# Performance work log

Hardware: AMD Instinct MI355X
Metric: run time of the kernel (lower is better)

## Reference

```python
import jax, jax.numpy as jnp
import numpy as np
import math

B, L, C = 16, 4096, 512
SPARSE_RATIO = 0.6
NUM_KEEP = math.ceil(L * SPARSE_RATIO)  # 2458


def setup_inputs() -> dict:
    key = jax.random.key(0)
    k1, k2, k3 = jax.random.split(key, 3)
    return {
        "tokens": jax.random.normal(k1, (B, L, C), dtype=jnp.float32),
        "attention_x": jax.random.normal(k2, (B, L), dtype=jnp.float32),
        "attention_y": jax.random.normal(k3, (B, L), dtype=jnp.float32),
    }


def reference(tokens, attention_x, attention_y):
    eps = 1e-6
    # coverage-fused score: alpha = sigmoid(1 - mean(ay)/mean(ax))
    coverage = attention_y.mean(axis=1) / (attention_x.mean(axis=1) + eps)  # [B]
    alpha = jax.nn.sigmoid(1.0 - coverage)                                  # [B]
    beta = 1.0 - alpha
    score = alpha[:, None] * attention_x + beta[:, None] * attention_y      # [B, L]

    # full descending sort of scores
    order = jnp.argsort(-score, axis=1)                                     # [B, L]
    score_sort = jnp.take_along_axis(score, order, axis=1)                  # [B, L]

    keep_policy = order[:, :NUM_KEEP]                                       # [B, K]
    non_keep_policy = order[:, NUM_KEEP:]                                   # [B, L-K]

    # scatter 1s at kept positions
    batch_idx = jnp.arange(B)[:, None]
    score_mask = jnp.zeros_like(score).at[batch_idx, keep_policy].set(1.0)  # [B, L]

    # gather kept / pruned tokens
    select_tokens = jnp.take_along_axis(tokens, keep_policy[:, :, None], axis=1)      # [B, K, C]
    non_tokens = jnp.take_along_axis(tokens, non_keep_policy[:, :, None], axis=1)     # [B, L-K, C]

    # softmax-weighted merge of pruned tokens into one extra token
    non_keep_score = jax.nn.softmax(score_sort[:, NUM_KEEP:], axis=1)[:, :, None]     # [B, L-K, 1]
    extra_token = jnp.sum(non_tokens * non_keep_score, axis=1, keepdims=True)         # [B, 1, C]

    return select_tokens, extra_token, score_mask
```

## Files before the change

### kernel.cpp

```cpp
#include <hip/hip_runtime.h>
#include <math.h>

#define NB 16
#define NL 4096
#define NC 512
#define NC4 128
#define NKEEP 2458
#define KEEPB 76
#define NTAILB 52

typedef float f32x4 __attribute__((ext_vector_type(4)));


__global__ void __launch_bounds__(1024) k_front(const float* __restrict__ ax,
                                                const float* __restrict__ ay,
                                                unsigned long long* __restrict__ key,
                                                float* __restrict__ alpha,
                                                float* __restrict__ beta,
                                                unsigned* __restrict__ smaxu) {
  int b = blockIdx.x;
  int tid = threadIdx.x;
  __shared__ float s_ab[2];
  __shared__ unsigned redmaxu[16];
  if (tid < 64) {
    int lane = tid;
    float sx = 0.0f, sy = 0.0f;
    if (lane < 32) {
      const float* px = ax + b * NL + lane * 128;
      const float* py = ay + b * NL + lane * 128;
      float r[8], q[8];
#pragma unroll
      for (int j = 0; j < 8; ++j) { r[j] = px[j]; q[j] = py[j]; }
      for (int i = 8; i < 128; i += 8) {
#pragma unroll
        for (int j = 0; j < 8; ++j) {
          r[j] = __fadd_rn(r[j], px[i + j]);
          q[j] = __fadd_rn(q[j], py[i + j]);
        }
      }
      sx = __fadd_rn(__fadd_rn(__fadd_rn(r[0], r[1]), __fadd_rn(r[2], r[3])),
                     __fadd_rn(__fadd_rn(r[4], r[5]), __fadd_rn(r[6], r[7])));
      sy = __fadd_rn(__fadd_rn(__fadd_rn(q[0], q[1]), __fadd_rn(q[2], q[3])),
                     __fadd_rn(__fadd_rn(q[4], q[5]), __fadd_rn(q[6], q[7])));
    }
#pragma unroll
    for (int m = 1; m <= 16; m <<= 1) {
      sx = __fadd_rn(sx, __shfl_xor(sx, m, 64));
      sy = __fadd_rn(sy, __shfl_xor(sy, m, 64));
    }
    if (lane == 0) {
      float mx = __fdiv_rn(sx, 4096.0f);
      float my = __fdiv_rn(sy, 4096.0f);
      float cov = __fdiv_rn(my, __fadd_rn(mx, 1e-6f));
      float z = __fsub_rn(1.0f, cov);
      double a = 1.0 / (1.0 + exp(-(double)z));
      float af = (float)a;
      alpha[b] = af;
      beta[b] = __fsub_rn(1.0f, af);
      s_ab[0] = af;
      s_ab[1] = __fsub_rn(1.0f, af);
    }
  }
  __syncthreads();
  float af = s_ab[0], bf = s_ab[1];
  unsigned m = 0;
#pragma unroll
  for (int p = 0; p < 4; ++p) {
    int l = p * 1024 + tid;
    int idx = b * NL + l;
    float s = __fadd_rn(__fmul_rn(af, ax[idx]), __fmul_rn(bf, ay[idx]));
    unsigned u = __float_as_uint(s);
    unsigned su = u ^ ((u & 0x80000000u) ? 0xFFFFFFFFu : 0x80000000u);
    key[idx] = ((unsigned long long)(~su) << 32) | (unsigned)l;
    m = (su > m) ? su : m;
  }
#pragma unroll
  for (int d = 1; d < 64; d <<= 1) {
    unsigned o = (unsigned)__shfl_xor((int)m, d, 64);
    m = (o > m) ? o : m;
  }
  if ((tid & 63) == 0) redmaxu[tid >> 6] = m;
  __syncthreads();
  if (tid == 0) {
    unsigned M = redmaxu[0];
#pragma unroll
    for (int k = 1; k < 16; ++k) M = (redmaxu[k] > M) ? redmaxu[k] : M;
    smaxu[b] = M;
  }
}

__global__ void __launch_bounds__(256) k_sort(const unsigned long long* __restrict__ key,
                                              unsigned long long* __restrict__ skey) {
  __shared__ unsigned long long lk[512];
  int b = blockIdx.y;
  int c = blockIdx.x;
  int t = threadIdx.x;
  const unsigned long long* kb = key + (size_t)b * NL + c * 512;
  lk[t] = kb[t];
  lk[t + 256] = kb[t + 256];
  __syncthreads();
  for (int k = 2; k <= 512; k <<= 1) {
    for (int j = k >> 1; j > 0; j >>= 1) {
#pragma unroll
      for (int e = 0; e < 2; ++e) {
        int i = t + e * 256;
        int l = i ^ j;
        if (l > i) {
          unsigned long long a = lk[i], bb = lk[l];
          bool up = ((i & k) == 0);
          if ((a > bb) == up) { lk[i] = bb; lk[l] = a; }
        }
      }
      __syncthreads();
    }
  }
  unsigned long long* sb = skey + ((size_t)b * 8 + c) * 512;
  sb[t] = lk[t];
  sb[t + 256] = lk[t + 256];
}

__global__ void __launch_bounds__(1024) k_mid(const float* __restrict__ ax,
                                              const float* __restrict__ ay,
                                              const float* __restrict__ alpha,
                                              const float* __restrict__ beta,
                                              const unsigned long long* __restrict__ skey,
                                              const unsigned* __restrict__ smaxu,
                                              float* __restrict__ w,
                                              float* __restrict__ mask_out,
                                              int* __restrict__ order,
                                              float* __restrict__ Zpart) {
  __shared__ unsigned long long lsk[4096];
  __shared__ float zred[16];
  int bx = blockIdx.x;
  int b = bx >> 2;
  int q = bx & 3;
  int t = threadIdx.x;
  const unsigned long long* sb = skey + (size_t)b * NL;
#pragma unroll
  for (int k = 0; k < 4; ++k) lsk[k * 1024 + t] = sb[k * 1024 + t];
  __syncthreads();

  int l = q * 1024 + t;
  int gid = b * NL + l;
  float s = __fadd_rn(__fmul_rn(alpha[b], ax[gid]), __fmul_rn(beta[b], ay[gid]));
  unsigned u = __float_as_uint(s);
  unsigned su = u ^ ((u & 0x80000000u) ? 0xFFFFFFFFu : 0x80000000u);
  unsigned long long ki = ((unsigned long long)(~su) << 32) | (unsigned)l;

  int r = 0;
#pragma unroll
  for (int c = 0; c < 8; ++c) {
    const unsigned long long* base = lsk + c * 512;
    int pos = 0;
#pragma unroll
    for (int step = 512; step >= 1; step >>= 1) {
      int cand = pos + step;
      if (cand <= 512 && base[cand - 1] < ki) pos = cand;
    }
    r += pos;
  }

  mask_out[gid] = (r < NKEEP) ? 1.0f : 0.0f;
  unsigned SU = smaxu[b];
  float smax = (SU & 0x80000000u) ? __uint_as_float(SU ^ 0x80000000u)
                                  : __uint_as_float(~SU);
  float wi = (r >= NKEEP) ? expf(s - smax) : 0.0f;
  w[gid] = wi;
  order[b * NL + r] = l;

  float zs = wi;
#pragma unroll
  for (int d = 1; d < 64; d <<= 1) zs += __shfl_xor(zs, d, 64);
  if ((t & 63) == 0) zred[t >> 6] = zs;
  __syncthreads();
  if (t == 0) {
    float z = 0.0f;
#pragma unroll
    for (int k = 0; k < 16; ++k) z += zred[k];
    Zpart[bx] = z;
  }
}

__global__ void __launch_bounds__(256) k_perm(const f32x4* __restrict__ tok,
                                              const int* __restrict__ order,
                                              const float* __restrict__ w,
                                              f32x4* __restrict__ sel,
                                              f32x4* __restrict__ partial) {
  int b = blockIdx.y;
  int bx = blockIdx.x;
  int p0 = bx * 32;
  int tid = threadIdx.x;
  int col = tid & 127;
  int g = tid >> 7;
  __shared__ int ssrc[32];
  __shared__ float swt[32];
  __shared__ float accsh[512];
  if (tid < 32) {
    int p = p0 + tid;
    int src = order[b * NL + p];
    ssrc[tid] = src;
    swt[tid] = w[b * NL + src];
  }
  __syncthreads();

  const f32x4* tb = tok + (size_t)b * NL * NC4 + col;
  f32x4 v[16];
#pragma unroll
  for (int k = 0; k < 16; ++k)
    v[k] = tb[(size_t)ssrc[g * 16 + k] * NC4];

  f32x4* sb = sel + (size_t)b * NKEEP * NC4 + col;
  float a0 = 0.f, a1 = 0.f, a2 = 0.f, a3 = 0.f;
#pragma unroll
  for (int k = 0; k < 16; ++k) {
    int p = p0 + g * 16 + k;
    if (p < NKEEP) {
      sb[(size_t)p * NC4] = v[k];
    } else {
      float wk = swt[g * 16 + k];
      a0 = fmaf(wk, v[k].x, a0);
      a1 = fmaf(wk, v[k].y, a1);
      a2 = fmaf(wk, v[k].z, a2);
      a3 = fmaf(wk, v[k].w, a3);
    }
  }

  if (bx >= KEEPB) {
    if (g == 1) {
      accsh[col * 4 + 0] = a0; accsh[col * 4 + 1] = a1;
      accsh[col * 4 + 2] = a2; accsh[col * 4 + 3] = a3;
    }
    __syncthreads();
    if (g == 0) {
      f32x4 o;
      o.x = a0 + accsh[col * 4 + 0];
      o.y = a1 + accsh[col * 4 + 1];
      o.z = a2 + accsh[col * 4 + 2];
      o.w = a3 + accsh[col * 4 + 3];
      partial[(size_t)(b * NTAILB + (bx - KEEPB)) * 128 + col] = o;
    }
  }
}

__global__ void __launch_bounds__(512) k_back(const float* __restrict__ partial,
                                              const float* __restrict__ Zpart,
                                              float* __restrict__ extra) {
  int b = blockIdx.x;
  int c = threadIdx.x;
  float Zb = 0.0f;
#pragma unroll
  for (int k = 0; k < 4; ++k) Zb += Zpart[b * 4 + k];
  const float* p = partial + (size_t)b * NTAILB * 512 + c;
  float a0 = 0.f, a1 = 0.f, a2 = 0.f, a3 = 0.f;
#pragma unroll
  for (int j = 0; j < NTAILB; j += 4) {
    a0 += p[(size_t)(j + 0) * 512];
    a1 += p[(size_t)(j + 1) * 512];
    a2 += p[(size_t)(j + 2) * 512];
    a3 += p[(size_t)(j + 3) * 512];
  }
  extra[b * NC + c] = ((a0 + a1) + (a2 + a3)) / Zb;
}

extern "C" void kernel_launch(void* const* d_in, const int* in_sizes, int n_in,
                              void* d_out, int out_size, void* d_ws, size_t ws_size,
                              hipStream_t stream) {
  (void)in_sizes; (void)n_in; (void)out_size; (void)ws_size;
  const f32x4* tok = (const f32x4*)d_in[0];
  const float* ax = (const float*)d_in[1];
  const float* ay = (const float*)d_in[2];

  unsigned long long* key = (unsigned long long*)d_ws;
  unsigned long long* skey = (unsigned long long*)((char*)d_ws + 524288);
  float* w = (float*)((char*)d_ws + 1048576);
  int* order = (int*)((char*)d_ws + 1310720);
  f32x4* partial = (f32x4*)((char*)d_ws + 1572864);
  float* scalars = (float*)((char*)d_ws + 3407872);
  float* alpha = scalars;
  float* beta = scalars + 16;
  unsigned* smaxu = (unsigned*)(scalars + 32);
  float* Zpart = scalars + 48;

  float* out = (float*)d_out;
  f32x4* sel = (f32x4*)out;
  float* extra = out + (size_t)NB * NKEEP * NC;
  float* mask = extra + (size_t)NB * NC;

  k_front<<<NB, 1024, 0, stream>>>(ax, ay, key, alpha, beta, smaxu);
  k_sort<<<dim3(8, NB), 256, 0, stream>>>(key, skey);
  k_mid<<<64, 1024, 0, stream>>>(ax, ay, alpha, beta, skey, smaxu, w, mask, order, Zpart);
  k_perm<<<dim3(128, NB), 256, 0, stream>>>(tok, order, w, sel, partial);
  k_back<<<NB, 512, 0, stream>>>((const float*)partial, Zpart, extra);
}
```

Baseline: 67.55 us.

## Fuse score computation into sort kernel and recompute alpha/max in mid kernel

Removes the separate k_front kernel. Each sort block now recomputes the per-batch alpha/beta from the attention means and builds its keys directly in shared memory, which drops a kernel launch and the global key round trip. The mid kernel recomputes alpha and takes the score max from the heads of the sorted chunks instead of a stored reduction. It also runs 128 blocks of 512 threads instead of 64 of 1024. In exchange the mean reduction is repeated in every block (8x per batch in each kernel), which adds redundant reads of ax and ay.

```diff
diff --git a/kernel.cpp b/kernel.cpp
--- a/kernel.cpp
+++ b/kernel.cpp
@@ -12,18 +12,17 @@
 typedef float f32x4 __attribute__((ext_vector_type(4)));
 
 
-__global__ void __launch_bounds__(1024) k_front(const float* __restrict__ ax,
-                                                const float* __restrict__ ay,
-                                                unsigned long long* __restrict__ key,
-                                                float* __restrict__ alpha,
-                                                float* __restrict__ beta,
-                                                unsigned* __restrict__ smaxu) {
-  int b = blockIdx.x;
-  int tid = threadIdx.x;
+__global__ void __launch_bounds__(256) k_sort(const float* __restrict__ ax,
+                                              const float* __restrict__ ay,
+                                              unsigned long long* __restrict__ skey) {
+  __shared__ unsigned long long lk[512];
   __shared__ float s_ab[2];
-  __shared__ unsigned redmaxu[16];
-  if (tid < 64) {
-    int lane = tid;
+  int b = blockIdx.y;
+  int c = blockIdx.x;
+  int t = threadIdx.x;
+
+  if (t < 64) {
+    int lane = t;
     float sx = 0.0f, sy = 0.0f;
     if (lane < 32) {
       const float* px = ax + b * NL + lane * 128;
@@ -55,50 +54,24 @@
       float z = __fsub_rn(1.0f, cov);
       double a = 1.0 / (1.0 + exp(-(double)z));
       float af = (float)a;
-      alpha[b] = af;
-      beta[b] = __fsub_rn(1.0f, af);
       s_ab[0] = af;
       s_ab[1] = __fsub_rn(1.0f, af);
     }
   }
   __syncthreads();
   float af = s_ab[0], bf = s_ab[1];
-  unsigned m = 0;
-#pragma unroll
-  for (int p = 0; p < 4; ++p) {
-    int l = p * 1024 + tid;
+
+#pragma unroll
+  for (int e = 0; e < 2; ++e) {
+    int l = c * 512 + t + e * 256;
     int idx = b * NL + l;
     float s = __fadd_rn(__fmul_rn(af, ax[idx]), __fmul_rn(bf, ay[idx]));
     unsigned u = __float_as_uint(s);
     unsigned su = u ^ ((u & 0x80000000u) ? 0xFFFFFFFFu : 0x80000000u);
-    key[idx] = ((unsigned long long)(~su) << 32) | (unsigned)l;
-    m = (su > m) ? su : m;
-  }
-#pragma unroll
-  for (int d = 1; d < 64; d <<= 1) {
-    unsigned o = (unsigned)__shfl_xor((int)m, d, 64);
-    m = (o > m) ? o : m;
-  }
-  if ((tid & 63) == 0) redmaxu[tid >> 6] = m;
-  __syncthreads();
-  if (tid == 0) {
-    unsigned M = redmaxu[0];
-#pragma unroll
-    for (int k = 1; k < 16; ++k) M = (redmaxu[k] > M) ? redmaxu[k] : M;
-    smaxu[b] = M;
-  }
-}
-
-__global__ void __launch_bounds__(256) k_sort(const unsigned long long* __restrict__ key,
-                                              unsigned long long* __restrict__ skey) {
-  __shared__ unsigned long long lk[512];
-  int b = blockIdx.y;
-  int c = blockIdx.x;
-  int t = threadIdx.x;
-  const unsigned long long* kb = key + (size_t)b * NL + c * 512;
-  lk[t] = kb[t];
-  lk[t + 256] = kb[t + 256];
-  __syncthreads();
+    lk[t + e * 256] = ((unsigned long long)(~su) << 32) | (unsigned)l;
+  }
+  __syncthreads();
+
   for (int k = 2; k <= 512; k <<= 1) {
     for (int j = k >> 1; j > 0; j >>= 1) {
 #pragma unroll
@@ -119,30 +92,76 @@
   sb[t + 256] = lk[t + 256];
 }
 
-__global__ void __launch_bounds__(1024) k_mid(const float* __restrict__ ax,
-                                              const float* __restrict__ ay,
-                                              const float* __restrict__ alpha,
-                                              const float* __restrict__ beta,
-                                              const unsigned long long* __restrict__ skey,
-                                              const unsigned* __restrict__ smaxu,
-                                              float* __restrict__ w,
-                                              float* __restrict__ mask_out,
-                                              int* __restrict__ order,
-                                              float* __restrict__ Zpart) {
+__global__ void __launch_bounds__(512) k_mid(const float* __restrict__ ax,
+                                             const float* __restrict__ ay,
+                                             const unsigned long long* __restrict__ skey,
+                                             float* __restrict__ w,
+                                             float* __restrict__ mask_out,
+                                             int* __restrict__ order,
+                                             float* __restrict__ Zpart) {
   __shared__ unsigned long long lsk[4096];
-  __shared__ float zred[16];
+  __shared__ float zred[8];
   int bx = blockIdx.x;
-  int b = bx >> 2;
-  int q = bx & 3;
+  int b = bx >> 3;
+  int q = bx & 7;
   int t = threadIdx.x;
   const unsigned long long* sb = skey + (size_t)b * NL;
 #pragma unroll
-  for (int k = 0; k < 4; ++k) lsk[k * 1024 + t] = sb[k * 1024 + t];
-  __syncthreads();
-
-  int l = q * 1024 + t;
+  for (int k = 0; k < 8; ++k) lsk[k * 512 + t] = sb[k * 512 + t];
+  __syncthreads();
+
+  unsigned long long kmin = lsk[0];
+#pragma unroll
+  for (int c = 1; c < 8; ++c) {
+    unsigned long long h = lsk[c * 512];
+    kmin = (h < kmin) ? h : kmin;
+  }
+  unsigned su0 = ~(unsigned)(kmin >> 32);
+  float smax = (su0 & 0x80000000u) ? __uint_as_float(su0 ^ 0x80000000u)
+                                   : __uint_as_float(~su0);
+
+  int l = q * 512 + t;
   int gid = b * NL + l;
-  float s = __fadd_rn(__fmul_rn(alpha[b], ax[gid]), __fmul_rn(beta[b], ay[gid]));
+  __shared__ float s_ab[2];
+  if (t < 64) {
+    int lane = t;
+    float sx = 0.0f, sy = 0.0f;
+    if (lane < 32) {
+      const float* px = ax + b * NL + lane * 128;
+      const float* py = ay + b * NL + lane * 128;
+      float r[8], qq[8];
+#pragma unroll
+      for (int j = 0; j < 8; ++j) { r[j] = px[j]; qq[j] = py[j]; }
+      for (int i = 8; i < 128; i += 8) {
+#pragma unroll
+        for (int j = 0; j < 8; ++j) {
+          r[j] = __fadd_rn(r[j], px[i + j]);
+          qq[j] = __fadd_rn(qq[j], py[i + j]);
+        }
+      }
+      sx = __fadd_rn(__fadd_rn(__fadd_rn(r[0], r[1]), __fadd_rn(r[2], r[3])),
+                     __fadd_rn(__fadd_rn(r[4], r[5]), __fadd_rn(r[6], r[7])));
+      sy = __fadd_rn(__fadd_rn(__fadd_rn(qq[0], qq[1]), __fadd_rn(qq[2], qq[3])),
+                     __fadd_rn(__fadd_rn(qq[4], qq[5]), __fadd_rn(qq[6], qq[7])));
+    }
+#pragma unroll
+    for (int m = 1; m <= 16; m <<= 1) {
+      sx = __fadd_rn(sx, __shfl_xor(sx, m, 64));
+      sy = __fadd_rn(sy, __shfl_xor(sy, m, 64));
+    }
+    if (lane == 0) {
+      float mx = __fdiv_rn(sx, 4096.0f);
+      float my = __fdiv_rn(sy, 4096.0f);
+      float cov = __fdiv_rn(my, __fadd_rn(mx, 1e-6f));
+      float z = __fsub_rn(1.0f, cov);
+      double a = 1.0 / (1.0 + exp(-(double)z));
+      float af = (float)a;
+      s_ab[0] = af;
+      s_ab[1] = __fsub_rn(1.0f, af);
+    }
+  }
+  __syncthreads();
+  float s = __fadd_rn(__fmul_rn(s_ab[0], ax[gid]), __fmul_rn(s_ab[1], ay[gid]));
   unsigned u = __float_as_uint(s);
   unsigned su = u ^ ((u & 0x80000000u) ? 0xFFFFFFFFu : 0x80000000u);
   unsigned long long ki = ((unsigned long long)(~su) << 32) | (unsigned)l;
@@ -161,9 +180,6 @@
   }
 
   mask_out[gid] = (r < NKEEP) ? 1.0f : 0.0f;
-  unsigned SU = smaxu[b];
-  float smax = (SU & 0x80000000u) ? __uint_as_float(SU ^ 0x80000000u)
-                                  : __uint_as_float(~SU);
   float wi = (r >= NKEEP) ? expf(s - smax) : 0.0f;
   w[gid] = wi;
   order[b * NL + r] = l;
@@ -176,7 +192,7 @@
   if (t == 0) {
     float z = 0.0f;
 #pragma unroll
-    for (int k = 0; k < 16; ++k) z += zred[k];
+    for (int k = 0; k < 8; ++k) z += zred[k];
     Zpart[bx] = z;
   }
 }
@@ -249,7 +265,7 @@
   int c = threadIdx.x;
   float Zb = 0.0f;
 #pragma unroll
-  for (int k = 0; k < 4; ++k) Zb += Zpart[b * 4 + k];
+  for (int k = 0; k < 8; ++k) Zb += Zpart[b * 8 + k];
   const float* p = partial + (size_t)b * NTAILB * 512 + c;
   float a0 = 0.f, a1 = 0.f, a2 = 0.f, a3 = 0.f;
 #pragma unroll
@@ -270,25 +286,19 @@
   const float* ax = (const float*)d_in[1];
   const float* ay = (const float*)d_in[2];
 
-  unsigned long long* key = (unsigned long long*)d_ws;
-  unsigned long long* skey = (unsigned long long*)((char*)d_ws + 524288);
-  float* w = (float*)((char*)d_ws + 1048576);
-  int* order = (int*)((char*)d_ws + 1310720);
-  f32x4* partial = (f32x4*)((char*)d_ws + 1572864);
-  float* scalars = (float*)((char*)d_ws + 3407872);
-  float* alpha = scalars;
-  float* beta = scalars + 16;
-  unsigned* smaxu = (unsigned*)(scalars + 32);
-  float* Zpart = scalars + 48;
+  unsigned long long* skey = (unsigned long long*)d_ws;
+  float* w = (float*)((char*)d_ws + 524288);
+  int* order = (int*)((char*)d_ws + 786432);
+  f32x4* partial = (f32x4*)((char*)d_ws + 1048576);
+  float* Zpart = (float*)((char*)d_ws + 2883584);
 
   float* out = (float*)d_out;
   f32x4* sel = (f32x4*)out;
   float* extra = out + (size_t)NB * NKEEP * NC;
   float* mask = extra + (size_t)NB * NC;
 
-  k_front<<<NB, 1024, 0, stream>>>(ax, ay, key, alpha, beta, smaxu);
-  k_sort<<<dim3(8, NB), 256, 0, stream>>>(key, skey);
-  k_mid<<<64, 1024, 0, stream>>>(ax, ay, alpha, beta, skey, smaxu, w, mask, order, Zpart);
+  k_sort<<<dim3(8, NB), 256, 0, stream>>>(ax, ay, skey);
+  k_mid<<<128, 512, 0, stream>>>(ax, ay, skey, w, mask, order, Zpart);
   k_perm<<<dim3(128, NB), 256, 0, stream>>>(tok, order, w, sel, partial);
   k_back<<<NB, 512, 0, stream>>>((const float*)partial, Zpart, extra);
 }
```

New measurement: 63.90 us. 1.06x faster.
